# Kernel optimization log

Hardware: AMD Instinct MI355X
Metric: run time of the kernel (lower is better)

## Reference

```python
import jax, jax.numpy as jnp
import numpy as np

WS = (8, 8)          # window_size
HEADS = 8
DH = 64              # dim_head
SHIFT = (4, 4)
SCALE = DH ** -0.5


def setup_inputs() -> dict:
    key = jax.random.key(0)
    ks = jax.random.split(key, 5)
    dim = 64
    inner = HEADS * DH  # 512
    b, h, w = 4, 192, 192
    x = jax.random.normal(ks[0], (b, h, w, dim), dtype=jnp.float32)
    Wq = jax.random.normal(ks[1], (dim, inner), dtype=jnp.float32) * (dim ** -0.5)
    Wkv = jax.random.normal(ks[2], (dim, 2 * inner), dtype=jnp.float32) * (dim ** -0.5)
    Wo = jax.random.normal(ks[3], (inner, dim), dtype=jnp.float32) * (inner ** -0.5)
    bo = jnp.zeros((dim,), dtype=jnp.float32)
    seq_l = WS[0] * WS[1]
    pos_emb = jax.random.normal(ks[4], (1, HEADS, seq_l, seq_l), dtype=jnp.float32)
    return {"x": x, "Wq": Wq, "Wkv": Wkv, "Wo": Wo, "bo": bo, "pos_emb": pos_emb}


def reference(x, Wq, Wkv, Wo, bo, pos_emb):
    b, h, w, c = x.shape
    L = WS[0] * WS[1]  # 64 tokens per window
    if SHIFT[0] > 0:
        x = jnp.roll(x, shift=(-SHIFT[0], -SHIFT[1]), axis=(1, 2))
    # NOTE: original uses a raw .view() here (row-major reshape), NOT an 8x8
    # window partition. Replicate exactly.
    nw = b * (h // WS[0]) * (w // WS[1])
    x_inp = x.reshape(nw, L, c)                      # [nw, 64, c]
    q = x_inp @ Wq                                   # [nw, 64, inner]
    kv = x_inp @ Wkv
    k, v = jnp.split(kv, 2, axis=-1)
    # original: raw view (nw, L, inner) -> (nw, heads, L, dh) (not a transpose)
    q = q.reshape(nw, HEADS, L, DH) * SCALE
    k = k.reshape(nw, HEADS, L, DH)
    v = v.reshape(nw, HEADS, L, DH)
    sim = jnp.einsum('bhid,bhjd->bhij', q, k) + pos_emb
    attn = jax.nn.softmax(sim, axis=-1)
    out = jnp.einsum('bhij,bhjd->bhid', attn, v)     # [nw, heads, 64, dh]
    # original: raw view back to (nw, L, inner)
    out = out.reshape(nw, L, HEADS * DH)
    out = out @ Wo + bo                              # [nw, 64, c]
    out = out.reshape(b, h, w, c)
    if SHIFT[0] > 0:
        out = jnp.roll(out, shift=(SHIFT[0], SHIFT[1]), axis=(1, 2))
    return out
```

## Files before the change

kernel.cpp:

```cpp
#include <hip/hip_runtime.h>
#include <stdint.h>

typedef __attribute__((ext_vector_type(8))) short bf16x8;
typedef __attribute__((ext_vector_type(4))) short s16x4;
typedef __attribute__((ext_vector_type(4))) float f32x4;

#define THREADS 256
constexpr int NWIN = 2304;

constexpr int WCATT_E = 0;
constexpr int WOT_E   = 98304;
constexpr int POS_E   = 131072;
constexpr size_t WS_NEED = 327680;

__device__ __forceinline__ short f2bf(float f) {
  uint32_t u = __builtin_bit_cast(uint32_t, f);
  u += 0x7fffu + ((u >> 16) & 1u);
  return (short)(u >> 16);
}
__device__ __forceinline__ float bf2f(short s) {
  uint32_t u = ((uint32_t)(uint16_t)s) << 16;
  return __builtin_bit_cast(float, u);
}
__device__ __forceinline__ int swz(int row, int h) {
  return ((((row ^ (row >> 2) ^ (row >> 3)) & 7) ^ h) << 4);
}

__global__ void wmsa_prep(const float* __restrict__ Wq, const float* __restrict__ Wkv,
                          const float* __restrict__ Wo, const float* __restrict__ pos,
                          short* __restrict__ ws) {
  int idx = blockIdx.x * 256 + threadIdx.x;
  if (idx < 32768) {
    int n = idx & 511, k = idx >> 9;
    ws[WCATT_E + n * 64 + k] = f2bf(Wq[k * 512 + n]);
  } else if (idx < 98304) {
    int j = idx - 32768;
    int nkv = j & 1023, k = j >> 10;
    ws[WCATT_E + (512 + nkv) * 64 + k] = f2bf(Wkv[k * 1024 + nkv]);
  } else if (idx < 131072) {
    int j = idx - 98304;
    int n = j & 63, k = j >> 6;
    ws[WOT_E + n * 512 + k] = f2bf(Wo[k * 64 + n]);
  } else if (idx < 163840) {
    int j = idx - 131072;
    ws[POS_E + j] = f2bf(pos[j]);
  }
}

__global__ __launch_bounds__(THREADS, 2)
void wmsa_mfma(const float* __restrict__ x, const float* __restrict__ bo,
               const short* __restrict__ ws, float* __restrict__ out) {
  __shared__ __align__(16) char lds[65536];
  const int tid = threadIdx.x;
  const int wv = tid >> 6;
  const int l  = tid & 63;
  const int lr = l & 15;
  const int lg = l >> 4;

  const int bid = blockIdx.x;
  const int p   = bid >> 2;
  const int hp  = bid & 3;

  const float* xrow[2];
  float* orow[2];
  int ww0a[2];
  #pragma unroll
  for (int win = 0; win < 2; ++win) {
    int w   = 2 * p + win;
    int t0  = w * 64;
    int bb  = t0 / 36864;
    int rem = t0 % 36864;
    int hh  = rem / 192;
    ww0a[win] = rem % 192;
    int src_h = (hh + 4) % 192;
    xrow[win] = x + (size_t)(bb * 192 + src_h) * 12288;
    orow[win] = out + (size_t)(bb * 192 + src_h) * 12288;
  }

  bf16x8 xa[2][2];
  #pragma unroll
  for (int win = 0; win < 2; ++win) {
    int tok = 16 * hp + lr;
    int sw = ww0a[win] + tok + 4; if (sw >= 192) sw -= 192;
    const float* xp = xrow[win] + sw * 64;
    #pragma unroll
    for (int ks = 0; ks < 2; ++ks) {
      float4 a = *(const float4*)(xp + ks * 32 + lg * 8);
      float4 b = *(const float4*)(xp + ks * 32 + lg * 8 + 4);
      bf16x8 v;
      v[0] = f2bf(a.x); v[1] = f2bf(a.y); v[2] = f2bf(a.z); v[3] = f2bf(a.w);
      v[4] = f2bf(b.x); v[5] = f2bf(b.y); v[6] = f2bf(b.z); v[7] = f2bf(b.w);
      xa[win][ks] = v;
    }
  }

  #pragma unroll 4
  for (int t = 0; t < 16; ++t) {
    int nt = wv + 4 * t;
    int nload = nt * 16 + lr;
    bf16x8 b0 = *(const bf16x8*)(ws + WCATT_E + nload * 64 + lg * 8);
    bf16x8 b1 = *(const bf16x8*)(ws + WCATT_E + nload * 64 + 32 + lg * 8);
    const bool isQ = (t < 8);
    int i  = (lr & 7) * 8 + (t & 7);
    int h2 = lr >> 3;
    int d0 = wv * 16 + lg * 4;
    int off = (isQ ? 0 : 16384) + h2 * 8192 + i * 128 + ((d0 * 2) ^ swz(i, h2));
    #pragma unroll
    for (int win = 0; win < 2; ++win) {
      f32x4 acc = {0.f, 0.f, 0.f, 0.f};
      acc = __builtin_amdgcn_mfma_f32_16x16x32_bf16(b0, xa[win][0], acc, 0, 0, 0);
      acc = __builtin_amdgcn_mfma_f32_16x16x32_bf16(b1, xa[win][1], acc, 0, 0, 0);
      s16x4 pk;
      if (isQ) {
        #pragma unroll
        for (int r = 0; r < 4; ++r) pk[r] = f2bf(acc[r] * 0.125f);
      } else {
        #pragma unroll
        for (int r = 0; r < 4; ++r) pk[r] = f2bf(acc[r]);
      }
      *(s16x4*)(lds + win * 32768 + off) = pk;
    }
  }
  __syncthreads();

  const int hl = wv >> 1;
  const int ih = wv & 1;
  const int hglob = 2 * hp + hl;

  s16x4 posr[2][4];
  #pragma unroll
  for (int it = 0; it < 2; ++it) {
    int i = (ih * 2 + it) * 16 + lr;
    const short* pp = ws + POS_E + hglob * 4096 + i * 64;
    #pragma unroll
    for (int jt = 0; jt < 4; ++jt)
      posr[it][jt] = *(const s16x4*)(pp + jt * 16 + lg * 4);
  }

  f32x4 vacc[2][8];
  #pragma unroll
  for (int tv = 0; tv < 8; ++tv) {
    int nload = (64 + wv + 4 * tv) * 16 + lr;
    bf16x8 b0 = *(const bf16x8*)(ws + WCATT_E + nload * 64 + lg * 8);
    bf16x8 b1 = *(const bf16x8*)(ws + WCATT_E + nload * 64 + 32 + lg * 8);
    #pragma unroll
    for (int win = 0; win < 2; ++win) {
      f32x4 acc = {0.f, 0.f, 0.f, 0.f};
      acc = __builtin_amdgcn_mfma_f32_16x16x32_bf16(xa[win][0], b0, acc, 0, 0, 0);
      acc = __builtin_amdgcn_mfma_f32_16x16x32_bf16(xa[win][1], b1, acc, 0, 0, 0);
      vacc[win][tv] = acc;
    }
  }

  #pragma unroll
  for (int win = 0; win < 2; ++win) {
    char* ldw = lds + win * 32768;
    f32x4 s[2][4];
    #pragma unroll
    for (int it = 0; it < 2; ++it)
      #pragma unroll
      for (int jt = 0; jt < 4; ++jt) s[it][jt] = (f32x4){0.f, 0.f, 0.f, 0.f};

    #pragma unroll
    for (int ks = 0; ks < 2; ++ks) {
      bf16x8 kb[4], qa[2];
      #pragma unroll
      for (int jt = 0; jt < 4; ++jt) {
        int j = jt * 16 + lr;
        kb[jt] = *(const bf16x8*)(ldw + 16384 + hl * 8192 + j * 128 + ((ks * 64 + lg * 16) ^ swz(j, hl)));
      }
      #pragma unroll
      for (int it = 0; it < 2; ++it) {
        int i = (ih * 2 + it) * 16 + lr;
        qa[it] = *(const bf16x8*)(ldw + hl * 8192 + i * 128 + ((ks * 64 + lg * 16) ^ swz(i, hl)));
      }
      #pragma unroll
      for (int it = 0; it < 2; ++it)
        #pragma unroll
        for (int jt = 0; jt < 4; ++jt)
          s[it][jt] = __builtin_amdgcn_mfma_f32_16x16x32_bf16(kb[jt], qa[it], s[it][jt], 0, 0, 0);
    }

    #pragma unroll
    for (int it = 0; it < 2; ++it) {
      int i = (ih * 2 + it) * 16 + lr;
      float sum = 0.f;
      #pragma unroll
      for (int jt = 0; jt < 4; ++jt)
        #pragma unroll
        for (int r = 0; r < 4; ++r) {
          float pv = __expf(s[it][jt][r] + bf2f(posr[it][jt][r]));
          s[it][jt][r] = pv;
          sum += pv;
        }
      sum += __shfl_xor(sum, 16);
      sum += __shfl_xor(sum, 32);
      float rinv = 1.f / sum;
      #pragma unroll
      for (int jt = 0; jt < 4; ++jt) {
        s16x4 pk;
        #pragma unroll
        for (int r = 0; r < 4; ++r) pk[r] = f2bf(s[it][jt][r] * rinv);
        *(s16x4*)(ldw + hl * 8192 + i * 128 + ((jt * 32 + lg * 8) ^ swz(i, hl))) = pk;
      }
    }
  }
  __syncthreads();

  {
    int d = wv * 16 + lr;
    #pragma unroll
    for (int win = 0; win < 2; ++win)
      #pragma unroll
      for (int r = 0; r < 4; ++r) {
        int tl = lg * 4 + r;
        int h2 = tl >> 3;
        char* vbase = lds + win * 32768 + 16384 + h2 * 8192 + d * 128;
        int slb = (tl & 7) * 16;
        #pragma unroll
        for (int g = 0; g < 2; ++g) {
          s16x4 pk;
          #pragma unroll
          for (int u = 0; u < 4; ++u) pk[u] = f2bf(vacc[win][4 * g + u][r]);
          *(s16x4*)(vbase + ((slb + 8 * g) ^ swz(d, h2))) = pk;
        }
      }
  }
  __syncthreads();

  #pragma unroll
  for (int win = 0; win < 2; ++win) {
    char* ldw = lds + win * 32768;
    f32x4 o[2][4];
    #pragma unroll
    for (int it = 0; it < 2; ++it)
      #pragma unroll
      for (int dt = 0; dt < 4; ++dt) o[it][dt] = (f32x4){0.f, 0.f, 0.f, 0.f};
    #pragma unroll
    for (int ks = 0; ks < 2; ++ks) {
      bf16x8 vb[4], pa[2];
      #pragma unroll
      for (int dt = 0; dt < 4; ++dt) {
        int d = dt * 16 + lr;
        vb[dt] = *(const bf16x8*)(ldw + 16384 + hl * 8192 + d * 128 + ((ks * 64 + lg * 16) ^ swz(d, hl)));
      }
      #pragma unroll
      for (int it = 0; it < 2; ++it) {
        int i = (ih * 2 + it) * 16 + lr;
        pa[it] = *(const bf16x8*)(ldw + hl * 8192 + i * 128 + ((ks * 64 + lg * 16) ^ swz(i, hl)));
      }
      #pragma unroll
      for (int it = 0; it < 2; ++it)
        #pragma unroll
        for (int dt = 0; dt < 4; ++dt)
          o[it][dt] = __builtin_amdgcn_mfma_f32_16x16x32_bf16(vb[dt], pa[it], o[it][dt], 0, 0, 0);
    }
    #pragma unroll
    for (int it = 0; it < 2; ++it) {
      int i  = (ih * 2 + it) * 16 + lr;
      int lm = 8 * hl + (i >> 3);
      int rp = lm * 8 + (i & 7);
      #pragma unroll
      for (int dt = 0; dt < 4; ++dt) {
        s16x4 pk;
        #pragma unroll
        for (int r = 0; r < 4; ++r) pk[r] = f2bf(o[it][dt][r]);
        *(s16x4*)(ldw + rp * 128 + ((dt * 32 + lg * 8) ^ swz(rp, 0))) = pk;
      }
    }
  }
  __syncthreads();

  f32x4 oacc[2];
  oacc[0] = (f32x4){0.f, 0.f, 0.f, 0.f};
  oacc[1] = (f32x4){0.f, 0.f, 0.f, 0.f};
  #pragma unroll 4
  for (int ks = 0; ks < 16; ++ks) {
    bf16x8 afrW = *(const bf16x8*)(ws + WOT_E + (wv * 16 + lr) * 512 + ks * 32 + lg * 8);
    int rp = lr * 8 + (ks >> 1);
    int boff = rp * 128 + (((ks & 1) * 64 + lg * 16) ^ swz(rp, 0));
    #pragma unroll
    for (int win = 0; win < 2; ++win) {
      bf16x8 bfrOH = *(const bf16x8*)(lds + win * 32768 + boff);
      oacc[win] = __builtin_amdgcn_mfma_f32_16x16x32_bf16(afrW, bfrOH, oacc[win], 0, 0, 0);
    }
  }
  {
    int c0 = wv * 16 + lg * 4;
    float4 bo4 = *(const float4*)(bo + c0);
    int tok = 16 * hp + lr;
    #pragma unroll
    for (int win = 0; win < 2; ++win) {
      int sw = ww0a[win] + tok + 4; if (sw >= 192) sw -= 192;
      float4 ov;
      ov.x = oacc[win][0] + bo4.x; ov.y = oacc[win][1] + bo4.y;
      ov.z = oacc[win][2] + bo4.z; ov.w = oacc[win][3] + bo4.w;
      *(float4*)(orow[win] + sw * 64 + c0) = ov;
    }
  }
}

constexpr float SCALEF = 0.125f;
constexpr int XSo = 0, Q8V = 4096, KT = 8256, SIMB = 12608, REDM = 16960, REDS = 17216, SMEMF = 17472;
__device__ __forceinline__ float f4c(const float4& v, int k) {
  return k == 0 ? v.x : k == 1 ? v.y : k == 2 ? v.z : v.w;
}
__global__ __launch_bounds__(THREADS, 2)
void wmsa_fp32(const float* __restrict__ x, const float* __restrict__ Wq,
               const float* __restrict__ Wkv, const float* __restrict__ Wo,
               const float* __restrict__ bo, const float* __restrict__ pos,
               float* __restrict__ out) {
  __shared__ float sm[SMEMF];
  const int tid = threadIdx.x;
  const int w   = blockIdx.x;
  const int t0  = w * 64;
  const int bb  = t0 / 36864;
  const int rem = t0 % 36864;
  const int hh  = rem / 192;
  const int ww0 = rem % 192;
  const int src_h = (hh + 4) % 192;
  const float* xrow = x + (size_t)(bb * 192 + src_h) * 12288;
  float* orow = out + (size_t)(bb * 192 + src_h) * 12288;
  for (int u = tid; u < 1024; u += THREADS) {
    int tok = u >> 4, c4 = (u & 15) << 2;
    int sw = ww0 + tok + 4; if (sw >= 192) sw -= 192;
    *reinterpret_cast<float4*>(&sm[XSo + tok * 64 + c4]) =
        *reinterpret_cast<const float4*>(xrow + sw * 64 + c4);
  }
  __syncthreads();
  for (int h = 0; h < 8; ++h) {
    const float* xsrow = &sm[XSo + (8 * h) * 64];
    {
      float acc[4][8];
      for (int m = 0; m < 4; ++m) for (int r = 0; r < 8; ++r) acc[m][r] = 0.f;
      #pragma unroll 4
      for (int c = 0; c < 64; ++c) {
        float xv[8];
        #pragma unroll
        for (int r = 0; r < 8; ++r) xv[r] = xsrow[r * 64 + c];
        #pragma unroll
        for (int m = 0; m < 4; ++m) {
          int jg = tid + 256 * m;
          float wv = (m < 2) ? Wq[c * 512 + jg] : Wkv[c * 1024 + (jg - 512)];
          #pragma unroll
          for (int r = 0; r < 8; ++r) acc[m][r] += xv[r] * wv;
        }
      }
      for (int m = 0; m < 2; ++m) { int qc = tid + 256 * m;
        for (int r = 0; r < 8; ++r) sm[Q8V + r * 520 + qc] = acc[m][r] * SCALEF; }
      for (int m = 2; m < 4; ++m) { int kc = tid + 256 * m - 512;
        int d = kc & 63, jh = kc >> 6;
        for (int r = 0; r < 8; ++r) sm[KT + d * 68 + 8 * r + jh] = acc[m][r]; }
    }
    __syncthreads();
    const int i0 = (tid >> 4) << 2;
    const int j0 = (tid & 15) << 2;
    {
      float s4[4][4];
      for (int a = 0; a < 4; ++a) for (int b = 0; b < 4; ++b) s4[a][b] = 0.f;
      #pragma unroll 2
      for (int dc = 0; dc < 64; dc += 4) {
        float4 q4[4], k4[4];
        #pragma unroll
        for (int a = 0; a < 4; ++a) { int i = i0 + a;
          q4[a] = *reinterpret_cast<const float4*>(&sm[Q8V + (i >> 3) * 520 + ((i & 7) << 6) + dc]); }
        #pragma unroll
        for (int dd = 0; dd < 4; ++dd)
          k4[dd] = *reinterpret_cast<const float4*>(&sm[KT + (dc + dd) * 68 + j0]);
        #pragma unroll
        for (int a = 0; a < 4; ++a)
          #pragma unroll
          for (int dd = 0; dd < 4; ++dd) {
            float qv = f4c(q4[a], dd);
            s4[a][0] += qv * k4[dd].x; s4[a][1] += qv * k4[dd].y;
            s4[a][2] += qv * k4[dd].z; s4[a][3] += qv * k4[dd].w;
          }
      }
      #pragma unroll
      for (int a = 0; a < 4; ++a) {
        float4 pv = *reinterpret_cast<const float4*>(&pos[((h * 64 + i0 + a) << 6) + j0]);
        float4 oo;
        oo.x = s4[a][0] + pv.x; oo.y = s4[a][1] + pv.y;
        oo.z = s4[a][2] + pv.z; oo.w = s4[a][3] + pv.w;
        *reinterpret_cast<float4*>(&sm[SIMB + (i0 + a) * 68 + j0]) = oo;
      }
    }
    __syncthreads();
    {
      float va[2][8];
      for (int m = 0; m < 2; ++m) for (int r = 0; r < 8; ++r) va[m][r] = 0.f;
      #pragma unroll 4
      for (int c = 0; c < 64; ++c) {
        float xv[8];
        #pragma unroll
        for (int r = 0; r < 8; ++r) xv[r] = xsrow[r * 64 + c];
        #pragma unroll
        for (int m = 0; m < 2; ++m) {
          float wv = Wkv[c * 1024 + 512 + tid + 256 * m];
          #pragma unroll
          for (int r = 0; r < 8; ++r) va[m][r] += xv[r] * wv;
        }
      }
      for (int m = 0; m < 2; ++m) { int vc = tid + 256 * m;
        for (int r = 0; r < 8; ++r) sm[Q8V + r * 520 + vc] = va[m][r]; }
    }
    {
      const int i = tid & 63, seg = tid >> 6;
      float* srow = &sm[SIMB + i * 68 + seg * 16];
      float mloc = -1e30f;
      #pragma unroll
      for (int u = 0; u < 16; ++u) mloc = fmaxf(mloc, srow[u]);
      sm[REDM + i * 4 + seg] = mloc;
      __syncthreads();
      float mrow = fmaxf(fmaxf(sm[REDM + i * 4 + 0], sm[REDM + i * 4 + 1]),
                         fmaxf(sm[REDM + i * 4 + 2], sm[REDM + i * 4 + 3]));
      float ssum = 0.f;
      #pragma unroll
      for (int u = 0; u < 16; ++u) {
        float p = __expf(srow[u] - mrow); srow[u] = p; ssum += p;
      }
      sm[REDS + i * 4 + seg] = ssum;
    }
    __syncthreads();
    {
      float rinv[4];
      #pragma unroll
      for (int a = 0; a < 4; ++a) {
        const float* rs = &sm[REDS + (i0 + a) * 4];
        rinv[a] = 1.f / (rs[0] + rs[1] + rs[2] + rs[3]);
      }
      float o4[4][4];
      for (int a = 0; a < 4; ++a) for (int b = 0; b < 4; ++b) o4[a][b] = 0.f;
      #pragma unroll 2
      for (int j = 0; j < 64; ++j) {
        float4 v4 = *reinterpret_cast<const float4*>(&sm[Q8V + (j >> 3) * 520 + ((j & 7) << 6) + j0]);
        #pragma unroll
        for (int a = 0; a < 4; ++a) {
          float p = sm[SIMB + (i0 + a) * 68 + j];
          o4[a][0] += p * v4.x; o4[a][1] += p * v4.y;
          o4[a][2] += p * v4.z; o4[a][3] += p * v4.w;
        }
      }
      __syncthreads();
      #pragma unroll
      for (int a = 0; a < 4; ++a) {
        float4 oo;
        oo.x = o4[a][0] * rinv[a]; oo.y = o4[a][1] * rinv[a];
        oo.z = o4[a][2] * rinv[a]; oo.w = o4[a][3] * rinv[a];
        *reinterpret_cast<float4*>(&sm[KT + (i0 + a) * 64 + j0]) = oo;
      }
    }
    __syncthreads();
    {
      const int c = tid & 63;
      const int r2 = tid >> 6;
      float acc0 = bo[c], acc1 = bo[c];
      const float* ohp = &sm[KT];
      #pragma unroll 8
      for (int jj = 0; jj < 512; ++jj) {
        float wv = Wo[jj * 64 + c];
        int jh = jj >> 6, dd = jj & 63;
        acc0 += ohp[(8 * r2 + jh) * 64 + dd] * wv;
        acc1 += ohp[(8 * (r2 + 4) + jh) * 64 + dd] * wv;
      }
      int l0 = 8 * h + r2, l1 = l0 + 4;
      int sw0 = ww0 + l0 + 4; if (sw0 >= 192) sw0 -= 192;
      int sw1 = ww0 + l1 + 4; if (sw1 >= 192) sw1 -= 192;
      orow[(size_t)sw0 * 64 + c] = acc0;
      orow[(size_t)sw1 * 64 + c] = acc1;
    }
    __syncthreads();
  }
}

extern "C" void kernel_launch(void* const* d_in, const int* in_sizes, int n_in,
                              void* d_out, int out_size, void* d_ws, size_t ws_size,
                              hipStream_t stream) {
  const float* x    = (const float*)d_in[0];
  const float* Wq   = (const float*)d_in[1];
  const float* Wkv  = (const float*)d_in[2];
  const float* Wo   = (const float*)d_in[3];
  const float* bo   = (const float*)d_in[4];
  const float* pos  = (const float*)d_in[5];
  float* o = (float*)d_out;
  if (ws_size >= WS_NEED) {
    wmsa_prep<<<dim3(640), dim3(256), 0, stream>>>(Wq, Wkv, Wo, pos, (short*)d_ws);
    wmsa_mfma<<<dim3(NWIN * 2), dim3(THREADS), 0, stream>>>(x, bo, (const short*)d_ws, o);
  } else {
    wmsa_fp32<<<dim3(NWIN), dim3(THREADS), 0, stream>>>(x, Wq, Wkv, Wo, bo, pos, o);
  }
}
```

Measured before the change: 192.5 us.

## Use 512-thread blocks with one window per wave group in MFMA kernel

After: 247.4 us. 28.5% more time.

```diff
diff --git a/kernel.cpp b/kernel.cpp
--- a/kernel.cpp
+++ b/kernel.cpp
@@ -47,7 +47,7 @@
   }
 }
 
-__global__ __launch_bounds__(THREADS, 2)
+__global__ __launch_bounds__(512, 4)
 void wmsa_mfma(const float* __restrict__ x, const float* __restrict__ bo,
                const short* __restrict__ ws, float* __restrict__ out) {
   __shared__ __align__(16) char lds[65536];
@@ -94,16 +94,16 @@
     }
   }
 
-  #pragma unroll 4
-  for (int t = 0; t < 16; ++t) {
-    int nt = wv + 4 * t;
+  #pragma unroll
+  for (int t = 0; t < 8; ++t) {
+    int nt = wv + 8 * t;
     int nload = nt * 16 + lr;
     bf16x8 b0 = *(const bf16x8*)(ws + WCATT_E + nload * 64 + lg * 8);
     bf16x8 b1 = *(const bf16x8*)(ws + WCATT_E + nload * 64 + 32 + lg * 8);
-    const bool isQ = (t < 8);
-    int i  = (lr & 7) * 8 + (t & 7);
+    const bool isQ = (t < 4);
+    int i  = (lr & 7) * 8 + ((nt >> 2) & 7);
     int h2 = lr >> 3;
-    int d0 = wv * 16 + lg * 4;
+    int d0 = (nt & 3) * 16 + lg * 4;
     int off = (isQ ? 0 : 16384) + h2 * 8192 + i * 128 + ((d0 * 2) ^ swz(i, h2));
     #pragma unroll
     for (int win = 0; win < 2; ++win) {
@@ -123,9 +123,11 @@
   }
   __syncthreads();
 
-  const int hl = wv >> 1;
-  const int ih = wv & 1;
+  const int win2 = wv >> 2;
+  const int hl   = (wv >> 1) & 1;
+  const int ih   = wv & 1;
   const int hglob = 2 * hp + hl;
+  char* ldw = lds + win2 * 32768;
 
   s16x4 posr[2][4];
   #pragma unroll
@@ -137,24 +139,26 @@
       posr[it][jt] = *(const s16x4*)(pp + jt * 16 + lg * 4);
   }
 
-  f32x4 vacc[2][8];
-  #pragma unroll
-  for (int tv = 0; tv < 8; ++tv) {
-    int nload = (64 + wv + 4 * tv) * 16 + lr;
-    bf16x8 b0 = *(const bf16x8*)(ws + WCATT_E + nload * 64 + lg * 8);
-    bf16x8 b1 = *(const bf16x8*)(ws + WCATT_E + nload * 64 + 32 + lg * 8);
-    #pragma unroll
-    for (int win = 0; win < 2; ++win) {
-      f32x4 acc = {0.f, 0.f, 0.f, 0.f};
-      acc = __builtin_amdgcn_mfma_f32_16x16x32_bf16(xa[win][0], b0, acc, 0, 0, 0);
-      acc = __builtin_amdgcn_mfma_f32_16x16x32_bf16(xa[win][1], b1, acc, 0, 0, 0);
-      vacc[win][tv] = acc;
-    }
-  }
-
-  #pragma unroll
-  for (int win = 0; win < 2; ++win) {
-    char* ldw = lds + win * 32768;
+  f32x4 vacc[2][4];
+  {
+    const int bq = wv & 3, aq = wv >> 2;
+    #pragma unroll
+    for (int u = 0; u < 4; ++u) {
+      int ntile = (aq * 4 + u) * 4 + bq;
+      int nload = (64 + ntile) * 16 + lr;
+      bf16x8 b0 = *(const bf16x8*)(ws + WCATT_E + nload * 64 + lg * 8);
+      bf16x8 b1 = *(const bf16x8*)(ws + WCATT_E + nload * 64 + 32 + lg * 8);
+      #pragma unroll
+      for (int win = 0; win < 2; ++win) {
+        f32x4 acc = {0.f, 0.f, 0.f, 0.f};
+        acc = __builtin_amdgcn_mfma_f32_16x16x32_bf16(xa[win][0], b0, acc, 0, 0, 0);
+        acc = __builtin_amdgcn_mfma_f32_16x16x32_bf16(xa[win][1], b1, acc, 0, 0, 0);
+        vacc[win][u] = acc;
+      }
+    }
+  }
+
+  {
     f32x4 s[2][4];
     #pragma unroll
     for (int it = 0; it < 2; ++it)
@@ -208,29 +212,24 @@
   __syncthreads();
 
   {
-    int d = wv * 16 + lr;
+    int d = (wv & 3) * 16 + lr;
+    int a8 = (wv >> 2) * 8;
     #pragma unroll
     for (int win = 0; win < 2; ++win)
       #pragma unroll
       for (int r = 0; r < 4; ++r) {
         int tl = lg * 4 + r;
         int h2 = tl >> 3;
-        char* vbase = lds + win * 32768 + 16384 + h2 * 8192 + d * 128;
-        int slb = (tl & 7) * 16;
-        #pragma unroll
-        for (int g = 0; g < 2; ++g) {
-          s16x4 pk;
-          #pragma unroll
-          for (int u = 0; u < 4; ++u) pk[u] = f2bf(vacc[win][4 * g + u][r]);
-          *(s16x4*)(vbase + ((slb + 8 * g) ^ swz(d, h2))) = pk;
-        }
+        int j0b = (tl & 7) * 16 + a8;
+        s16x4 pk;
+        #pragma unroll
+        for (int u = 0; u < 4; ++u) pk[u] = f2bf(vacc[win][u][r]);
+        *(s16x4*)(lds + win * 32768 + 16384 + h2 * 8192 + d * 128 + (j0b ^ swz(d, h2))) = pk;
       }
   }
   __syncthreads();
 
-  #pragma unroll
-  for (int win = 0; win < 2; ++win) {
-    char* ldw = lds + win * 32768;
+  {
     f32x4 o[2][4];
     #pragma unroll
     for (int it = 0; it < 2; ++it)
@@ -271,32 +270,24 @@
   }
   __syncthreads();
 
-  f32x4 oacc[2];
-  oacc[0] = (f32x4){0.f, 0.f, 0.f, 0.f};
-  oacc[1] = (f32x4){0.f, 0.f, 0.f, 0.f};
-  #pragma unroll 4
-  for (int ks = 0; ks < 16; ++ks) {
-    bf16x8 afrW = *(const bf16x8*)(ws + WOT_E + (wv * 16 + lr) * 512 + ks * 32 + lg * 8);
-    int rp = lr * 8 + (ks >> 1);
-    int boff = rp * 128 + (((ks & 1) * 64 + lg * 16) ^ swz(rp, 0));
-    #pragma unroll
-    for (int win = 0; win < 2; ++win) {
-      bf16x8 bfrOH = *(const bf16x8*)(lds + win * 32768 + boff);
-      oacc[win] = __builtin_amdgcn_mfma_f32_16x16x32_bf16(afrW, bfrOH, oacc[win], 0, 0, 0);
-    }
-  }
   {
-    int c0 = wv * 16 + lg * 4;
+    f32x4 oacc = {0.f, 0.f, 0.f, 0.f};
+    const int ct = wv & 3;
+    #pragma unroll 4
+    for (int ks = 0; ks < 16; ++ks) {
+      bf16x8 afrW = *(const bf16x8*)(ws + WOT_E + (ct * 16 + lr) * 512 + ks * 32 + lg * 8);
+      int rp = lr * 8 + (ks >> 1);
+      bf16x8 bfrOH = *(const bf16x8*)(ldw + rp * 128 + (((ks & 1) * 64 + lg * 16) ^ swz(rp, 0)));
+      oacc = __builtin_amdgcn_mfma_f32_16x16x32_bf16(afrW, bfrOH, oacc, 0, 0, 0);
+    }
+    int c0 = ct * 16 + lg * 4;
     float4 bo4 = *(const float4*)(bo + c0);
     int tok = 16 * hp + lr;
-    #pragma unroll
-    for (int win = 0; win < 2; ++win) {
-      int sw = ww0a[win] + tok + 4; if (sw >= 192) sw -= 192;
-      float4 ov;
-      ov.x = oacc[win][0] + bo4.x; ov.y = oacc[win][1] + bo4.y;
-      ov.z = oacc[win][2] + bo4.z; ov.w = oacc[win][3] + bo4.w;
-      *(float4*)(orow[win] + sw * 64 + c0) = ov;
-    }
+    int sw = ww0a[win2] + tok + 4; if (sw >= 192) sw -= 192;
+    float4 ov;
+    ov.x = oacc[0] + bo4.x; ov.y = oacc[1] + bo4.y;
+    ov.z = oacc[2] + bo4.z; ov.w = oacc[3] + bo4.w;
+    *(float4*)(orow[win2] + sw * 64 + c0) = ov;
   }
 }
 
@@ -485,7 +476,7 @@
   float* o = (float*)d_out;
   if (ws_size >= WS_NEED) {
     wmsa_prep<<<dim3(640), dim3(256), 0, stream>>>(Wq, Wkv, Wo, pos, (short*)d_ws);
-    wmsa_mfma<<<dim3(NWIN * 2), dim3(THREADS), 0, stream>>>(x, bo, (const short*)d_ws, o);
+    wmsa_mfma<<<dim3(NWIN * 2), dim3(512), 0, stream>>>(x, bo, (const short*)d_ws, o);
   } else {
     wmsa_fp32<<<dim3(NWIN), dim3(THREADS), 0, stream>>>(x, Wq, Wkv, Wo, bo, pos, o);
   }
```
